# Performance work log

Hardware: AMD Instinct MI355X
Metric: run time of the kernel (lower is better)

## Reference

```python
import jax, jax.numpy as jnp
import numpy as np

DIM = 768
HEADS = 12
HEAD_DIM = DIM // HEADS  # 64
SCALE = HEAD_DIM ** -0.5
B, H, W = 16, 64, 64
EPS_BN = 1e-5
EPS_SQRT = 1e-5


def setup_inputs() -> dict:
    key = jax.random.key(0)
    k0, k1, k2, k3, k4 = jax.random.split(key, 5)
    x = jax.random.normal(k0, (B, DIM, H, W), dtype=jnp.float32)
    # 1x1 conv == pointwise matmul over channels
    qkv_w = jax.random.normal(k1, (3 * DIM, DIM), dtype=jnp.float32) * (DIM ** -0.5)
    qkv_b = jax.random.normal(k2, (3 * DIM,), dtype=jnp.float32) * 0.01
    gamma = 1.0 + 0.1 * jax.random.normal(k3, (DIM,), dtype=jnp.float32)
    beta = 0.1 * jax.random.normal(k4, (DIM,), dtype=jnp.float32)
    return {"x": x, "qkv_w": qkv_w, "qkv_b": qkv_b, "gamma": gamma, "beta": beta}


def reference(x, qkv_w, qkv_b, gamma, beta):
    b, c, h, w = x.shape
    n = h * w
    xf = x.reshape(b, c, n)  # [B, C, N]
    # qkv 1x1 conv
    qkv = jnp.einsum('oc,bcn->bon', qkv_w, xf) + qkv_b[None, :, None]  # [B, 3C, N]
    qkv = qkv.reshape(b, 3, HEADS, HEAD_DIM, n)
    q, k, v = qkv[:, 0], qkv[:, 1], qkv[:, 2]  # each [B, h, d, N]
    # channel attention: contract over N -> [B, h, d, d]
    attn = jnp.einsum('bhdn,bhen->bhde', q, k) * SCALE
    attn = jnp.sign(attn) * jnp.sqrt(jnp.abs(attn) + EPS_SQRT)
    attn = jax.nn.softmax(attn, axis=-1)
    # BatchNorm2d (training-mode batch statistics, biased variance) + ReLU
    mean = jnp.mean(x, axis=(0, 2, 3))
    var = jnp.var(x, axis=(0, 2, 3))
    y = (x - mean[None, :, None, None]) * jax.lax.rsqrt(var + EPS_BN)[None, :, None, None]
    y = y * gamma[None, :, None, None] + beta[None, :, None, None]
    out = jnp.maximum(y, 0.0)
    # original module discards attn; returned here so the attention math is
    return out, attn
```

## Files before the change

### kernel.cpp

```cpp
#include <hip/hip_runtime.h>
#include <hip/hip_bf16.h>

#define DIM 768
#define NB 16
#define NPOS 4096
#define HEADS 12

typedef unsigned short u16;
typedef __attribute__((ext_vector_type(4))) float f32x4;
typedef __attribute__((ext_vector_type(8))) short s16x8;
typedef __attribute__((ext_vector_type(4))) u16 u16x4;

static __device__ __forceinline__ u16 f2bf(float f) {
  __hip_bfloat16 h = __float2bfloat16(f);
  u16 u; __builtin_memcpy(&u, &h, 2); return u;
}
static __device__ __forceinline__ float bf2f(u16 u) {
  unsigned int x = ((unsigned int)u) << 16;
  float f; __builtin_memcpy(&f, &x, 4); return f;
}

static __device__ __forceinline__ void load_lds16(const void* g, void* l) {
  __builtin_amdgcn_global_load_lds(
      (const __attribute__((address_space(1))) unsigned int*)g,
      (__attribute__((address_space(3))) unsigned int*)l, 16, 0, 0);
}

static __device__ __forceinline__ int lds_idx(int row, int slotf) {
  return row * 64 + (((slotf) ^ (row & 7)) << 3);
}


__global__ __launch_bounds__(128) void sums_cast_kernel(const float* __restrict__ x,
                                                        float* __restrict__ sum_bc,
                                                        float* __restrict__ sumsq_bc,
                                                        u16* __restrict__ Xb) {
  int bc = blockIdx.x;
  const float4* p = (const float4*)(x + (size_t)bc * NPOS);
  u16x4* ob = (u16x4*)(Xb + (size_t)bc * NPOS);
  int t = threadIdx.x;
  float s = 0.f, ss = 0.f;
  for (int i = t; i < NPOS / 4; i += 128) {
    float4 v = p[i];
    s  += v.x + v.y + v.z + v.w;
    ss += v.x * v.x + v.y * v.y + v.z * v.z + v.w * v.w;
    u16x4 hv = {f2bf(v.x), f2bf(v.y), f2bf(v.z), f2bf(v.w)};
    ob[i] = hv;
  }
  for (int off = 32; off; off >>= 1) { s += __shfl_down(s, off); ss += __shfl_down(ss, off); }
  __shared__ float red[4];
  int lane = t & 63, w = t >> 6;
  if (lane == 0) { red[w] = s; red[2 + w] = ss; }
  __syncthreads();
  if (t == 0) { sum_bc[bc] = red[0] + red[1]; sumsq_bc[bc] = red[2] + red[3]; }
}

__global__ void finalize_kernel(const float* __restrict__ sum_bc, const float* __restrict__ sumsq_bc,
                                const float* __restrict__ gamma, const float* __restrict__ beta,
                                float* __restrict__ chanScale, float* __restrict__ chanShift) {
  int c = blockIdx.x * blockDim.x + threadIdx.x;
  if (c >= DIM) return;
  float s = 0.f, ss = 0.f;
  for (int b = 0; b < NB; b++) { s += sum_bc[b * DIM + c]; ss += sumsq_bc[b * DIM + c]; }
  const float invn = 1.f / ((float)NB * (float)NPOS);
  float mean = s * invn;
  float var  = ss * invn - mean * mean;
  float rstd = rsqrtf(var + 1e-5f);
  float a = rstd * gamma[c];
  chanScale[c] = a;
  chanShift[c] = beta[c] - mean * a;
}

__global__ __launch_bounds__(256) void bn_kernel(const float* __restrict__ x,
                                                 const float* __restrict__ chanScale,
                                                 const float* __restrict__ chanShift,
                                                 float* __restrict__ out) {
  const size_t n4 = (size_t)NB * DIM * NPOS / 4;
  const float4* x4 = (const float4*)x;
  float4* o4 = (float4*)out;
  for (size_t i = (size_t)blockIdx.x * blockDim.x + threadIdx.x; i < n4;
       i += (size_t)gridDim.x * blockDim.x) {
    float4 v = x4[i];
    int c = (int)((i >> 10) % DIM);
    float a = chanScale[c], sh = chanShift[c];
    v.x = fmaxf(fmaf(v.x, a, sh), 0.f);
    v.y = fmaxf(fmaf(v.y, a, sh), 0.f);
    v.z = fmaxf(fmaf(v.z, a, sh), 0.f);
    v.w = fmaxf(fmaf(v.w, a, sh), 0.f);
    o4[i] = v;
  }
}


__global__ __launch_bounds__(64) void tvecw_kernel(const float* __restrict__ W,
                                                   const float* __restrict__ sum_bc,
                                                   float* __restrict__ tvec,
                                                   u16* __restrict__ Wb) {
  int r = blockIdx.x;
  int lane = threadIdx.x;
  const float* wr = W + (size_t)r * DIM;
  float acc[NB];
#pragma unroll
  for (int b = 0; b < NB; b++) acc[b] = 0.f;
#pragma unroll
  for (int j = 0; j < DIM / 64; j++) {
    int c = lane + j * 64;
    float wv = wr[c];
    Wb[(size_t)r * DIM + c] = f2bf(wv);
#pragma unroll
    for (int b = 0; b < NB; b++) acc[b] += wv * sum_bc[b * DIM + c];
  }
#pragma unroll
  for (int b = 0; b < NB; b++) {
    float v = acc[b];
    for (int off = 32; off; off >>= 1) v += __shfl_down(v, off);
    if (lane == 0) tvec[(size_t)b * 1536 + r] = v;
  }
}


template <bool SYMM>
__global__ __launch_bounds__(256) void gemm_kernel(
    const u16* __restrict__ A, long long strideA,
    const u16* __restrict__ B, long long strideB,
    u16* __restrict__ C, long long strideC,
    int lda, int ldb, int ldc, int K, int nGram,
    const u16* __restrict__ XbBn, const float* __restrict__ chanScale,
    const float* __restrict__ chanShift, float* __restrict__ outY) {
  __shared__ __align__(16) u16 As[2][128 * 64];
  __shared__ __align__(16) u16 Bs[2][128 * 64];

  int ti, tj, bz;
  if (SYMM) {
    if ((int)blockIdx.x >= nGram) {
      int t = threadIdx.x;
      const size_t total8 = (size_t)NB * DIM * NPOS / 8;
      size_t stride = (size_t)(gridDim.x - nGram) * 256;
      const s16x8* xs = (const s16x8*)XbBn;
      float4* o4 = (float4*)outY;
      for (size_t i = (size_t)(blockIdx.x - nGram) * 256 + t; i < total8; i += stride) {
        s16x8 v = xs[i];
        int c = (int)((i >> 9) % DIM);
        float a = chanScale[c], sh = chanShift[c];
        float4 o0, o1;
        o0.x = fmaxf(fmaf(bf2f((u16)v[0]), a, sh), 0.f);
        o0.y = fmaxf(fmaf(bf2f((u16)v[1]), a, sh), 0.f);
        o0.z = fmaxf(fmaf(bf2f((u16)v[2]), a, sh), 0.f);
        o0.w = fmaxf(fmaf(bf2f((u16)v[3]), a, sh), 0.f);
        o1.x = fmaxf(fmaf(bf2f((u16)v[4]), a, sh), 0.f);
        o1.y = fmaxf(fmaf(bf2f((u16)v[5]), a, sh), 0.f);
        o1.z = fmaxf(fmaf(bf2f((u16)v[6]), a, sh), 0.f);
        o1.w = fmaxf(fmaf(bf2f((u16)v[7]), a, sh), 0.f);
        o4[2 * i] = o0;
        o4[2 * i + 1] = o1;
      }
      return;
    }
    int bid = blockIdx.x;
    int swz = (bid & 7) * 42 + (bid >> 3);
    bz = swz / 21;
    int idx = swz % 21, rem = 6;
    ti = 0;
    while (idx >= rem) { idx -= rem; ti++; rem--; }
    tj = ti + idx;
  } else {
    ti = blockIdx.x; tj = blockIdx.y; bz = blockIdx.z;
  }
  const u16* Ab = A + (size_t)bz * strideA;
  const u16* Bb = B + (size_t)bz * strideB;
  u16* Cb = C + (size_t)bz * strideC;
  int ib = ti * 128, jb = tj * 128;

  int t = threadIdx.x, lane = t & 63, w = t >> 6;
  int wr = (w >> 1) * 64, wc = (w & 1) * 64;
  int fr = lane & 15, q4 = lane >> 4;
  int srow = lane >> 3;
  int sslot = (lane & 7) ^ srow;

  const u16* Asrc = Ab + (size_t)(ib + srow) * lda + sslot * 8;
  const u16* Bsrc = Bb + (size_t)(jb + srow) * ldb + sslot * 8;

  f32x4 acc[4][4];
#pragma unroll
  for (int m = 0; m < 4; m++)
#pragma unroll
    for (int n = 0; n < 4; n++) acc[m][n] = (f32x4){0.f, 0.f, 0.f, 0.f};

#define STAGE(buf, k0)                                                          \
  {                                                                             \
    _Pragma("unroll")                                                           \
    for (int i = 0; i < 4; i++) {                                               \
      int q = w * 4 + i;             \
      load_lds16(Asrc + (size_t)(q * 8) * lda + (k0), (char*)As[buf] + q * 1024);\
      load_lds16(Bsrc + (size_t)(q * 8) * ldb + (k0), (char*)Bs[buf] + q * 1024);\
    }                                                                           \
  }

#define COMPUTE(buf)                                                            \
  {                                                                             \
    _Pragma("unroll")                                                           \
    for (int kk = 0; kk < 2; kk++) {                                            \
      int sbase = kk * 4 + q4;                                                  \
      s16x8 af[4], bfv[4];                                                      \
      _Pragma("unroll")                                                         \
      for (int m = 0; m < 4; m++) af[m] = *(const s16x8*)&As[buf][lds_idx(wr + m * 16 + fr, sbase)]; \
      _Pragma("unroll")                                                         \
      for (int n = 0; n < 4; n++) bfv[n] = *(const s16x8*)&Bs[buf][lds_idx(wc + n * 16 + fr, sbase)]; \
      _Pragma("unroll")                                                         \
      for (int m = 0; m < 4; m++)                                               \
        _Pragma("unroll")                                                       \
        for (int n = 0; n < 4; n++)                                             \
          acc[m][n] = __builtin_amdgcn_mfma_f32_16x16x32_bf16(af[m], bfv[n], acc[m][n], 0, 0, 0); \
    }                                                                           \
  }

  const int nt = K >> 6;
  STAGE(0, 0);
  for (int t2 = 0; t2 < nt; t2 += 2) {
    STAGE(1, (t2 + 1) << 6);
    asm volatile("s_waitcnt vmcnt(8)" ::: "memory");
    __builtin_amdgcn_s_barrier();
    __builtin_amdgcn_sched_barrier(0);
    COMPUTE(0);
    __builtin_amdgcn_s_barrier();
    if (t2 + 2 < nt) {
      STAGE(0, (t2 + 2) << 6);
      asm volatile("s_waitcnt vmcnt(8)" ::: "memory");
    } else {
      asm volatile("s_waitcnt vmcnt(0)" ::: "memory");
    }
    __builtin_amdgcn_s_barrier();
    __builtin_amdgcn_sched_barrier(0);
    COMPUTE(1);
    __builtin_amdgcn_s_barrier();
  }
#undef STAGE
#undef COMPUTE

  int rbase = q4 * 4;
#pragma unroll
  for (int m = 0; m < 4; m++)
#pragma unroll
    for (int n = 0; n < 4; n++)
#pragma unroll
      for (int r = 0; r < 4; r++) {
        int row = ib + wr + m * 16 + rbase + r;
        int col = jb + wc + n * 16 + fr;
        u16 v = f2bf(acc[m][n][r]);
        Cb[(size_t)row * ldc + col] = v;
        if (SYMM && ti != tj) Cb[(size_t)col * ldc + row] = v;
      }
}


__global__ __launch_bounds__(256) void attn_kernel(const u16* __restrict__ Pb,
                                                   const u16* __restrict__ Wb,
                                                   const float* __restrict__ bias,
                                                   const float* __restrict__ tvec,
                                                   float* __restrict__ outAttn) {
  int h = blockIdx.x, b = blockIdx.y;
  __shared__ __align__(16) u16 As[2][64 * 64];
  __shared__ __align__(16) u16 Bs[2][64 * 64];
  __shared__ float sm[64 * 65];
  const u16* Pa = Pb + ((size_t)b * DIM + h * 64) * DIM;
  const u16* Wk = Wb + (size_t)(DIM + h * 64) * DIM;

  int t = threadIdx.x, lane = t & 63, w = t >> 6;
  int fr = lane & 15, q4 = lane >> 4;
  int srow = lane >> 3;
  int sslot = (lane & 7) ^ srow;

  const u16* Asrc = Pa + (size_t)srow * DIM + sslot * 8;
  const u16* Bsrc = Wk + (size_t)srow * DIM + sslot * 8;

  f32x4 acc[4];
#pragma unroll
  for (int n = 0; n < 4; n++) acc[n] = (f32x4){0.f, 0.f, 0.f, 0.f};

#define ASTAGE(buf, k0)                                                          \
  {                                                                              \
    _Pragma("unroll")                                                            \
    for (int i = 0; i < 2; i++) {                                                \
      int q = w * 2 + i;              \
      load_lds16(Asrc + (size_t)(q * 8) * DIM + (k0), (char*)As[buf] + q * 1024);\
      load_lds16(Bsrc + (size_t)(q * 8) * DIM + (k0), (char*)Bs[buf] + q * 1024);\
    }                                                                            \
  }

#define ACOMPUTE(buf)                                                            \
  {                                                                              \
    _Pragma("unroll")                                                            \
    for (int kk = 0; kk < 2; kk++) {                                             \
      int sbase = kk * 4 + q4;                                                   \
      s16x8 af = *(const s16x8*)&As[buf][lds_idx(w * 16 + fr, sbase)];           \
      _Pragma("unroll")                                                          \
      for (int n = 0; n < 4; n++) {                                              \
        s16x8 bfv = *(const s16x8*)&Bs[buf][lds_idx(n * 16 + fr, sbase)];        \
        acc[n] = __builtin_amdgcn_mfma_f32_16x16x32_bf16(af, bfv, acc[n], 0, 0, 0); \
      }                                                                          \
    }                                                                            \
  }

  ASTAGE(0, 0);
  for (int t2 = 0; t2 < 12; t2 += 2) {
    ASTAGE(1, (t2 + 1) << 6);
    asm volatile("s_waitcnt vmcnt(4)" ::: "memory");
    __builtin_amdgcn_s_barrier();
    __builtin_amdgcn_sched_barrier(0);
    ACOMPUTE(0);
    __builtin_amdgcn_s_barrier();
    if (t2 + 2 < 12) {
      ASTAGE(0, (t2 + 2) << 6);
      asm volatile("s_waitcnt vmcnt(4)" ::: "memory");
    } else {
      asm volatile("s_waitcnt vmcnt(0)" ::: "memory");
    }
    __builtin_amdgcn_s_barrier();
    __builtin_amdgcn_sched_barrier(0);
    ACOMPUTE(1);
    __builtin_amdgcn_s_barrier();
  }
#undef ASTAGE
#undef ACOMPUTE

  const float* tq = tvec + (size_t)b * 1536 + h * 64;
  const float* tk = tq + DIM;
  const float* bq = bias + h * 64;
  const float* bk = bias + DIM + h * 64;
  int rbase = q4 * 4;
#pragma unroll
  for (int n = 0; n < 4; n++) {
    int e = n * 16 + fr;
    float bke = bk[e], tke = tk[e];
#pragma unroll
    for (int r = 0; r < 4; r++) {
      int d = w * 16 + rbase + r;
      float bqd = bq[d];
      float raw = acc[n][r] + bqd * tke + bke * tq[d] + 4096.f * bqd * bke;
      float val = 0.125f * raw;
      float sq = sqrtf(fabsf(val) + 1e-5f);
      sm[d * 65 + e] = val > 0.f ? sq : (val < 0.f ? -sq : 0.f);
    }
  }
  __syncthreads();
  {
    int d = t >> 2, qd = (t & 3) * 16;
    const float* row = &sm[d * 65];
    float mx = -1e30f;
#pragma unroll
    for (int e2 = 0; e2 < 16; e2++) mx = fmaxf(mx, row[qd + e2]);
    mx = fmaxf(mx, __shfl_xor(mx, 1));
    mx = fmaxf(mx, __shfl_xor(mx, 2));
    float sum = 0.f;
#pragma unroll
    for (int e2 = 0; e2 < 16; e2++) sum += __expf(row[qd + e2] - mx);
    sum += __shfl_xor(sum, 1);
    sum += __shfl_xor(sum, 2);
    float inv = 1.f / sum;
    float* o = outAttn + (((size_t)b * HEADS + h) * 64 + d) * 64;
#pragma unroll
    for (int e2 = 0; e2 < 16; e2++) o[qd + e2] = __expf(row[qd + e2] - mx) * inv;
  }
}


extern "C" void kernel_launch(void* const* d_in, const int* in_sizes, int n_in,
                              void* d_out, int out_size, void* d_ws, size_t ws_size,
                              hipStream_t stream) {
  const float* x     = (const float*)d_in[0];
  const float* qkv_w = (const float*)d_in[1];
  const float* qkv_b = (const float*)d_in[2];
  const float* gamma = (const float*)d_in[3];
  const float* beta  = (const float*)d_in[4];
  float* out = (float*)d_out;
  float* ws  = (float*)d_ws;

  float* sum_bc    = ws;
  float* sumsq_bc  = ws + 12288;
  float* chanScale = ws + 24576;
  float* chanShift = ws + 25344;
  float* tvec      = ws + 26112;
  u16* Wb = (u16*)(ws + 50688);
  u16* Gb = (u16*)((char*)d_ws + 2562048);
  u16* Pb = (u16*)((char*)d_ws + 2562048 + 18874368);

  const bool wsRoom = ws_size >= (41943040ull + 100663296ull + 1024ull);
  u16* Xb = wsRoom ? (u16*)((char*)d_ws + 41943040) : (u16*)d_out;

  sums_cast_kernel<<<NB * DIM, 128, 0, stream>>>(x, sum_bc, sumsq_bc, Xb);
  finalize_kernel<<<3, 256, 0, stream>>>(sum_bc, sumsq_bc, gamma, beta, chanScale, chanShift);
  tvecw_kernel<<<2 * DIM, 64, 0, stream>>>(qkv_w, sum_bc, tvec, Wb);

  if (wsRoom) {
    gemm_kernel<true><<<336 + 256, 256, 0, stream>>>(
        Xb, (long long)DIM * NPOS, Xb, (long long)DIM * NPOS, Gb, (long long)DIM * DIM,
        NPOS, NPOS, DIM, NPOS, 336, Xb, chanScale, chanShift, out);
  } else {
    gemm_kernel<true><<<336, 256, 0, stream>>>(
        Xb, (long long)DIM * NPOS, Xb, (long long)DIM * NPOS, Gb, (long long)DIM * DIM,
        NPOS, NPOS, DIM, NPOS, 336, nullptr, chanScale, chanShift, nullptr);
    bn_kernel<<<2048, 256, 0, stream>>>(x, chanScale, chanShift, out);
  }

  gemm_kernel<false><<<dim3(6, 6, NB), 256, 0, stream>>>(
      Wb, 0LL, Gb, (long long)DIM * DIM, Pb, (long long)DIM * DIM,
      DIM, DIM, DIM, DIM, 1 << 30, nullptr, nullptr, nullptr, nullptr);

  attn_kernel<<<dim3(HEADS, NB), 256, 0, stream>>>(Pb, Wb, qkv_b, tvec,
                                                   out + (size_t)NB * DIM * NPOS);
}
```

Measured before the change: 270.6 us.

## Replace direct global-to-LDS loads with register-staged prefetch pipeline in GEMM kernels

```diff
diff --git a/kernel.cpp b/kernel.cpp
--- a/kernel.cpp
+++ b/kernel.cpp
@@ -18,12 +18,6 @@
 static __device__ __forceinline__ float bf2f(u16 u) {
   unsigned int x = ((unsigned int)u) << 16;
   float f; __builtin_memcpy(&f, &x, 4); return f;
-}
-
-static __device__ __forceinline__ void load_lds16(const void* g, void* l) {
-  __builtin_amdgcn_global_load_lds(
-      (const __attribute__((address_space(1))) unsigned int*)g,
-      (__attribute__((address_space(3))) unsigned int*)l, 16, 0, 0);
 }
 
 static __device__ __forceinline__ int lds_idx(int row, int slotf) {
@@ -171,14 +165,17 @@
   u16* Cb = C + (size_t)bz * strideC;
   int ib = ti * 128, jb = tj * 128;
 
-  int t = threadIdx.x, lane = t & 63, w = t >> 6;
+  int t = threadIdx.x, lane = t & 63;
+  int w = t >> 6;
   int wr = (w >> 1) * 64, wc = (w & 1) * 64;
   int fr = lane & 15, q4 = lane >> 4;
-  int srow = lane >> 3;
-  int sslot = (lane & 7) ^ srow;
+  int srow = t >> 3;
+  int sslot = t & 7;
+  int wslot = sslot ^ (srow & 7);
 
   const u16* Asrc = Ab + (size_t)(ib + srow) * lda + sslot * 8;
   const u16* Bsrc = Bb + (size_t)(jb + srow) * ldb + sslot * 8;
+  int lw = srow * 64 + wslot * 8;
 
   f32x4 acc[4][4];
 #pragma unroll
@@ -186,13 +183,23 @@
 #pragma unroll
     for (int n = 0; n < 4; n++) acc[m][n] = (f32x4){0.f, 0.f, 0.f, 0.f};
 
-#define STAGE(buf, k0)                                                          \
-  {                                                                             \
-    _Pragma("unroll")                                                           \
-    for (int i = 0; i < 4; i++) {                                               \
-      int q = w * 4 + i;             \
-      load_lds16(Asrc + (size_t)(q * 8) * lda + (k0), (char*)As[buf] + q * 1024);\
-      load_lds16(Bsrc + (size_t)(q * 8) * ldb + (k0), (char*)Bs[buf] + q * 1024);\
+  s16x8 rA[4], rB[4];
+
+#define GLOAD(k0)                                                               \
+  {                                                                             \
+    _Pragma("unroll")                                                           \
+    for (int p = 0; p < 4; p++) {                                               \
+      rA[p] = *(const s16x8*)(Asrc + (size_t)(p * 32) * lda + (k0));            \
+      rB[p] = *(const s16x8*)(Bsrc + (size_t)(p * 32) * ldb + (k0));            \
+    }                                                                           \
+  }
+
+#define DSW(buf)                                                                \
+  {                                                                             \
+    _Pragma("unroll")                                                           \
+    for (int p = 0; p < 4; p++) {                                               \
+      *(s16x8*)&As[buf][lw + p * 2048] = rA[p];                                 \
+      *(s16x8*)&Bs[buf][lw + p * 2048] = rB[p];                                 \
     }                                                                           \
   }
 
@@ -215,26 +222,30 @@
   }
 
   const int nt = K >> 6;
-  STAGE(0, 0);
+  GLOAD(0);
+  DSW(0);
+  GLOAD(64);
+  asm volatile("s_waitcnt lgkmcnt(0)" ::: "memory");
+  __builtin_amdgcn_s_barrier();
+  __builtin_amdgcn_sched_barrier(0);
   for (int t2 = 0; t2 < nt; t2 += 2) {
-    STAGE(1, (t2 + 1) << 6);
-    asm volatile("s_waitcnt vmcnt(8)" ::: "memory");
-    __builtin_amdgcn_s_barrier();
-    __builtin_amdgcn_sched_barrier(0);
     COMPUTE(0);
-    __builtin_amdgcn_s_barrier();
-    if (t2 + 2 < nt) {
-      STAGE(0, (t2 + 2) << 6);
-      asm volatile("s_waitcnt vmcnt(8)" ::: "memory");
-    } else {
-      asm volatile("s_waitcnt vmcnt(0)" ::: "memory");
-    }
+    DSW(1);
+    if (t2 + 2 < nt) GLOAD((t2 + 2) << 6);
+    asm volatile("s_waitcnt lgkmcnt(0)" ::: "memory");
     __builtin_amdgcn_s_barrier();
     __builtin_amdgcn_sched_barrier(0);
     COMPUTE(1);
+    if (t2 + 2 < nt) {
+      DSW(0);
+      if (t2 + 3 < nt) GLOAD((t2 + 3) << 6);
+    }
+    asm volatile("s_waitcnt lgkmcnt(0)" ::: "memory");
     __builtin_amdgcn_s_barrier();
-  }
-#undef STAGE
+    __builtin_amdgcn_sched_barrier(0);
+  }
+#undef GLOAD
+#undef DSW
 #undef COMPUTE
 
   int rbase = q4 * 4;
@@ -267,60 +278,76 @@
 
   int t = threadIdx.x, lane = t & 63, w = t >> 6;
   int fr = lane & 15, q4 = lane >> 4;
-  int srow = lane >> 3;
-  int sslot = (lane & 7) ^ srow;
+  int srow = t >> 3;
+  int sslot = t & 7;
+  int wslot = sslot ^ (srow & 7);
 
   const u16* Asrc = Pa + (size_t)srow * DIM + sslot * 8;
   const u16* Bsrc = Wk + (size_t)srow * DIM + sslot * 8;
+  int lw = srow * 64 + wslot * 8;
 
   f32x4 acc[4];
 #pragma unroll
   for (int n = 0; n < 4; n++) acc[n] = (f32x4){0.f, 0.f, 0.f, 0.f};
 
-#define ASTAGE(buf, k0)                                                          \
-  {                                                                              \
-    _Pragma("unroll")                                                            \
-    for (int i = 0; i < 2; i++) {                                                \
-      int q = w * 2 + i;              \
-      load_lds16(Asrc + (size_t)(q * 8) * DIM + (k0), (char*)As[buf] + q * 1024);\
-      load_lds16(Bsrc + (size_t)(q * 8) * DIM + (k0), (char*)Bs[buf] + q * 1024);\
-    }                                                                            \
-  }
-
-#define ACOMPUTE(buf)                                                            \
-  {                                                                              \
-    _Pragma("unroll")                                                            \
-    for (int kk = 0; kk < 2; kk++) {                                             \
-      int sbase = kk * 4 + q4;                                                   \
-      s16x8 af = *(const s16x8*)&As[buf][lds_idx(w * 16 + fr, sbase)];           \
-      _Pragma("unroll")                                                          \
-      for (int n = 0; n < 4; n++) {                                              \
-        s16x8 bfv = *(const s16x8*)&Bs[buf][lds_idx(n * 16 + fr, sbase)];        \
+  s16x8 rA[2], rB[2];
+
+#define AGLOAD(k0)                                                              \
+  {                                                                             \
+    _Pragma("unroll")                                                           \
+    for (int p = 0; p < 2; p++) {                                               \
+      rA[p] = *(const s16x8*)(Asrc + (size_t)(p * 32) * DIM + (k0));            \
+      rB[p] = *(const s16x8*)(Bsrc + (size_t)(p * 32) * DIM + (k0));            \
+    }                                                                           \
+  }
+
+#define ADSW(buf)                                                               \
+  {                                                                             \
+    _Pragma("unroll")                                                           \
+    for (int p = 0; p < 2; p++) {                                               \
+      *(s16x8*)&As[buf][lw + p * 2048] = rA[p];                                 \
+      *(s16x8*)&Bs[buf][lw + p * 2048] = rB[p];                                 \
+    }                                                                           \
+  }
+
+#define ACOMPUTE(buf)                                                           \
+  {                                                                             \
+    _Pragma("unroll")                                                           \
+    for (int kk = 0; kk < 2; kk++) {                                            \
+      int sbase = kk * 4 + q4;                                                  \
+      s16x8 af = *(const s16x8*)&As[buf][lds_idx(w * 16 + fr, sbase)];          \
+      _Pragma("unroll")                                                         \
+      for (int n = 0; n < 4; n++) {                                             \
+        s16x8 bfv = *(const s16x8*)&Bs[buf][lds_idx(n * 16 + fr, sbase)];       \
         acc[n] = __builtin_amdgcn_mfma_f32_16x16x32_bf16(af, bfv, acc[n], 0, 0, 0); \
-      }                                                                          \
-    }                                                                            \
-  }
-
-  ASTAGE(0, 0);
+      }                                                                         \
+    }                                                                           \
+  }
+
+  AGLOAD(0);
+  ADSW(0);
+  AGLOAD(64);
+  asm volatile("s_waitcnt lgkmcnt(0)" ::: "memory");
+  __builtin_amdgcn_s_barrier();
+  __builtin_amdgcn_sched_barrier(0);
   for (int t2 = 0; t2 < 12; t2 += 2) {
-    ASTAGE(1, (t2 + 1) << 6);
-    asm volatile("s_waitcnt vmcnt(4)" ::: "memory");
-    __builtin_amdgcn_s_barrier();
-    __builtin_amdgcn_sched_barrier(0);
     ACOMPUTE(0);
-    __builtin_amdgcn_s_barrier();
-    if (t2 + 2 < 12) {
-      ASTAGE(0, (t2 + 2) << 6);
-      asm volatile("s_waitcnt vmcnt(4)" ::: "memory");
-    } else {
-      asm volatile("s_waitcnt vmcnt(0)" ::: "memory");
-    }
+    ADSW(1);
+    if (t2 + 2 < 12) AGLOAD((t2 + 2) << 6);
+    asm volatile("s_waitcnt lgkmcnt(0)" ::: "memory");
     __builtin_amdgcn_s_barrier();
     __builtin_amdgcn_sched_barrier(0);
     ACOMPUTE(1);
+    if (t2 + 2 < 12) {
+      ADSW(0);
+      if (t2 + 3 < 12) AGLOAD((t2 + 3) << 6);
+    }
+    asm volatile("s_waitcnt lgkmcnt(0)" ::: "memory");
     __builtin_amdgcn_s_barrier();
-  }
-#undef ASTAGE
+    __builtin_amdgcn_sched_barrier(0);
+  }
+#undef AGLOAD
+#undef ADSW
 #undef ACOMPUTE
 
   const float* tq = tvec + (size_t)b * 1536 + h * 64;
```

Measured after the change: 254.9 us, median of 2. 5.8% less time.
